# Kernel optimization log

Hardware: AMD Instinct MI355X
Metric: run time of the kernel (lower is better)

The kernel has to match this reference:

```python
import jax, jax.numpy as jnp
import numpy as np

ALPHA = 10.0 / 100.0  # dt / tau
HIDDEN_NOISE = 0.1
B, T, IN, H, OUT = 256, 200, 33, 2048, 4


def setup_inputs() -> dict:
    key = jax.random.key(0)
    k1, k2, k3, k4, k5 = jax.random.split(key, 5)
    x = jax.random.normal(k1, (B, T, IN), dtype=jnp.float32)
    # Pre-drawn per-step hidden noise (torch.normal(mean=0, std=hidden_noise)), shape [T, B, H]
    noise = jax.random.normal(k2, (T, B, H), dtype=jnp.float32) * HIDDEN_NOISE
    Wi2h = jax.random.normal(k3, (H, IN), dtype=jnp.float32) * (1.0 / np.sqrt(IN))
    Wrec = jax.random.normal(k4, (H, H), dtype=jnp.float32) * (1.0 / np.sqrt(H))
    Wh2o = jax.random.normal(k5, (OUT, H), dtype=jnp.float32) * (1.0 / np.sqrt(H))
    return {"x": x, "noise": noise, "Wi2h": Wi2h, "Wrec": Wrec, "Wh2o": Wh2o}


def reference(x, noise, Wi2h, Wrec, Wh2o):
    # x: [B, T, IN]; noise: [T, B, H]; Wi2h: [H, IN]; Wrec: [H, H]; Wh2o: [OUT, H]
    b = x.shape[0]
    # Input projection for all timesteps at once: it = i2h(x[:, t, :])
    it_all = jnp.einsum('bti,hi->tbh', x, Wi2h)  # [T, B, H]
    h0 = jnp.zeros((b, Wrec.shape[0]), dtype=x.dtype)

    def step(h_prev, inp):
        it, nz = inp
        pre = it + h_prev @ Wrec.T + nz
        h = jax.nn.relu(pre) * ALPHA + (1.0 - ALPHA) * h_prev  # external = 0, no ceiling
        out = jax.nn.softmax(h @ Wh2o.T, axis=1)
        return h, (h, out)

    _, (hs, outs) = jax.lax.scan(step, h0, (it_all, noise))
    hiddens = jnp.swapaxes(hs, 0, 1)   # [B, T, H]
    outs = jnp.swapaxes(outs, 0, 1)    # [B, T, OUT]
    return hiddens, outs
```

## Files before the change

### kernel.cpp

```cpp
#include <hip/hip_runtime.h>
#include <math.h>

#define Bq 256
#define Tq 200
#define INq 33
#define Hq 2048
#define OUTq 4

typedef __attribute__((ext_vector_type(8))) short bf16x8;
typedef __attribute__((ext_vector_type(16))) float f32x16;
typedef __attribute__((ext_vector_type(4))) unsigned short us4;

#define MFMA32(A, B, C) __builtin_amdgcn_mfma_f32_32x32x16_bf16((A), (B), (C), 0, 0, 0)

__device__ __forceinline__ unsigned short f32_to_bf16(float f) {
  unsigned u = __float_as_uint(f);
  unsigned r = 0x7FFFu + ((u >> 16) & 1u);
  return (unsigned short)((u + r) >> 16);
}
__device__ __forceinline__ float bf16_to_f32(unsigned short h) {
  return __uint_as_float((unsigned)h << 16);
}

#define WS_W1     0ull
#define WS_W2     8388608ull
#define WS_W3     16777216ull
#define WS_SLABF0 25165824ull
#define WS_SLABF1 27262976ull
#define WS_APARTS 29360128ull
#define WS_WIT    35651584ull
#define WS_TOTAL  35921920ull

#define DOT4(ACC, Av, Bv) \
  ACC = fmaf((Av).x, (Bv).x, ACC); ACC = fmaf((Av).y, (Bv).y, ACC); \
  ACC = fmaf((Av).z, (Bv).z, ACC); ACC = fmaf((Av).w, (Bv).w, ACC)

__global__ __launch_bounds__(256) void conv_wrec(
    const float* __restrict__ W, unsigned short* __restrict__ w1,
    unsigned short* __restrict__ w2, unsigned short* __restrict__ w3)
{
  const int g   = blockIdx.x * 256 + threadIdx.x;
  const int col = g >> 7;
  const int kc  = g & 127;
  const float* src = W + (size_t)col * Hq + kc * 16;
  unsigned short s1[16], s2[16], s3[16];
#pragma unroll
  for (int j = 0; j < 16; ++j) {
    float v = src[j];
    unsigned short b1 = f32_to_bf16(v);
    float r1 = v - bf16_to_f32(b1);
    unsigned short b2 = f32_to_bf16(r1);
    float r2 = r1 - bf16_to_f32(b2);
    s1[j] = b1; s2[j] = b2; s3[j] = f32_to_bf16(r2);
  }
  const size_t o_lo = ((size_t)(kc * 64 + (col >> 5)) * 64 + (col & 31)) * 8;
  const size_t o_hi = o_lo + 256;
#pragma unroll
  for (int jj = 0; jj < 2; ++jj) {
    *(us4*)&w1[o_lo + jj * 4] = *(us4*)&s1[jj * 4];
    *(us4*)&w1[o_hi + jj * 4] = *(us4*)&s1[8 + jj * 4];
    *(us4*)&w2[o_lo + jj * 4] = *(us4*)&s2[jj * 4];
    *(us4*)&w2[o_hi + jj * 4] = *(us4*)&s2[8 + jj * 4];
    *(us4*)&w3[o_lo + jj * 4] = *(us4*)&s3[jj * 4];
    *(us4*)&w3[o_hi + jj * 4] = *(us4*)&s3[8 + jj * 4];
  }
}

__global__ __launch_bounds__(256) void conv_wi(
    const float* __restrict__ Wi2h, float* __restrict__ WiT)
{
  const int g = blockIdx.x * 256 + threadIdx.x;
  if (g >= INq * Hq) return;
  const int i = g >> 11;
  const int c = g & 2047;
  WiT[(size_t)i * Hq + c] = Wi2h[(size_t)c * INq + i];
}

__global__ __launch_bounds__(256) void proj_tail(
    const float* __restrict__ hbase, size_t rstride,
    const float* __restrict__ Wh2o, float* __restrict__ out_o, int tp)
{
  const int tid = threadIdx.x;
  const int r  = blockIdx.x * 64 + (tid >> 2);
  const int p4 = tid & 3;
  const float* hp = hbase + (size_t)r * rstride;
  float a0 = 0.f, a1 = 0.f, a2 = 0.f, a3 = 0.f;
  const int k0 = p4 * 512;
#pragma unroll 4
  for (int k = k0; k < k0 + 512; k += 4) {
    float4 hv = *(const float4*)(hp + k);
    float4 w0 = *(const float4*)(Wh2o + 0 * Hq + k);
    float4 w1 = *(const float4*)(Wh2o + 1 * Hq + k);
    float4 w2 = *(const float4*)(Wh2o + 2 * Hq + k);
    float4 w3 = *(const float4*)(Wh2o + 3 * Hq + k);
    DOT4(a0, hv, w0); DOT4(a1, hv, w1); DOT4(a2, hv, w2); DOT4(a3, hv, w3);
  }
  a0 += __shfl_xor(a0, 1); a1 += __shfl_xor(a1, 1);
  a2 += __shfl_xor(a2, 1); a3 += __shfl_xor(a3, 1);
  a0 += __shfl_xor(a0, 2); a1 += __shfl_xor(a1, 2);
  a2 += __shfl_xor(a2, 2); a3 += __shfl_xor(a3, 2);
  if (p4 == 0) {
    float m  = fmaxf(fmaxf(a0, a1), fmaxf(a2, a3));
    float e0 = expf(a0 - m), e1 = expf(a1 - m);
    float e2 = expf(a2 - m), e3 = expf(a3 - m);
    float inv = 1.0f / (e0 + e1 + e2 + e3);
    float* op = out_o + ((size_t)r * Tq + tp) * OUTq;
    op[0] = e0 * inv; op[1] = e1 * inv; op[2] = e2 * inv; op[3] = e3 * inv;
  }
}

__global__ __launch_bounds__(512, 1) void rnn_step_mfma(
    const float* __restrict__ x, const float* __restrict__ noise,
    const float* __restrict__ WiT, const float* __restrict__ Wh2o,
    const unsigned short* __restrict__ w1, const unsigned short* __restrict__ w2,
    const unsigned short* __restrict__ w3,
    const float* __restrict__ hprevF,
    const unsigned short* __restrict__ a1, const unsigned short* __restrict__ a2,
    const unsigned short* __restrict__ a3,
    float* __restrict__ houtF,
    unsigned short* __restrict__ o1, unsigned short* __restrict__ o2,
    unsigned short* __restrict__ o3,
    float* __restrict__ out_h, float* __restrict__ out_o, int t)
{
  __shared__ float P[4 * 2176 + 32];

  const int wg  = blockIdx.x;
  const int tid = threadIdx.x;

  const int L  = (wg & 7) * 32 + (wg >> 3);
  const int TC = L >> 3;
  const int TR = L & 7;

  const int lane = tid & 63;
  const int wv   = __builtin_amdgcn_readfirstlane(tid >> 6);
  const int ct   = wv & 1;
  const int q    = wv >> 1;

  if (t > 0) {
    float* ps = P + 4 * 2176;
    const int i4 = tid * 4;
    float4 hv  = *(const float4*)(hprevF + (size_t)wg * Hq + i4);
    float4 q0v = *(const float4*)(Wh2o + 0 * Hq + i4);
    float4 q1v = *(const float4*)(Wh2o + 1 * Hq + i4);
    float4 q2v = *(const float4*)(Wh2o + 2 * Hq + i4);
    float4 q3v = *(const float4*)(Wh2o + 3 * Hq + i4);
    float s0 = 0.f, s1 = 0.f, s2 = 0.f, s3 = 0.f;
    DOT4(s0, hv, q0v); DOT4(s1, hv, q1v); DOT4(s2, hv, q2v); DOT4(s3, hv, q3v);
#pragma unroll
    for (int m = 1; m <= 32; m <<= 1) {
      s0 += __shfl_xor(s0, m); s1 += __shfl_xor(s1, m);
      s2 += __shfl_xor(s2, m); s3 += __shfl_xor(s3, m);
    }
    if ((tid & 63) == 0) {
      ps[wv * 4 + 0] = s0; ps[wv * 4 + 1] = s1;
      ps[wv * 4 + 2] = s2; ps[wv * 4 + 3] = s3;
    }
    __syncthreads();
    if (tid == 0) {
      float t0 = 0.f, t1 = 0.f, t2 = 0.f, t3 = 0.f;
#pragma unroll
      for (int w = 0; w < 8; ++w) {
        t0 += ps[w * 4 + 0]; t1 += ps[w * 4 + 1];
        t2 += ps[w * 4 + 2]; t3 += ps[w * 4 + 3];
      }
      float m  = fmaxf(fmaxf(t0, t1), fmaxf(t2, t3));
      float e0 = expf(t0 - m), e1 = expf(t1 - m);
      float e2 = expf(t2 - m), e3 = expf(t3 - m);
      float inv = 1.0f / (e0 + e1 + e2 + e3);
      float* op = out_o + ((size_t)wg * Tq + (t - 1)) * OUTq;
      op[0] = e0 * inv; op[1] = e1 * inv; op[2] = e2 * inv; op[3] = e3 * inv;
    }
    __syncthreads();
  }

  f32x16 accA, accB;
#pragma unroll
  for (int i = 0; i < 16; ++i) { accA[i] = 0.f; accB[i] = 0.f; }

  if (t > 0) {
    const int kc0 = q * 32;
    const unsigned short* pa1 = a1 + ((size_t)(kc0 * 8 + TR) * 64 + lane) * 8;
    const unsigned short* pa2 = a2 + ((size_t)(kc0 * 8 + TR) * 64 + lane) * 8;
    const unsigned short* pa3 = a3 + ((size_t)(kc0 * 8 + TR) * 64 + lane) * 8;
    const int cb = TC * 2 + ct;
    const unsigned short* pb1 = w1 + ((size_t)(kc0 * 64 + cb) * 64 + lane) * 8;
    const unsigned short* pb2 = w2 + ((size_t)(kc0 * 64 + cb) * 64 + lane) * 8;
    const unsigned short* pb3 = w3 + ((size_t)(kc0 * 64 + cb) * 64 + lane) * 8;

#define LA(P_, c) (*(const bf16x8*)((P_) + ((size_t)(c) << 12)))
#define LB(P_, c) (*(const bf16x8*)((P_) + ((size_t)(c) << 15)))
    bf16x8 A1x = LA(pa1, 0), A2x = LA(pa2, 0), A3x = LA(pa3, 0);
    bf16x8 B1x = LB(pb1, 0), B2x = LB(pb2, 0), B3x = LB(pb3, 0);
    bf16x8 A1y = LA(pa1, 1), A2y = LA(pa2, 1), A3y = LA(pa3, 1);
    bf16x8 B1y = LB(pb1, 1), B2y = LB(pb2, 1), B3y = LB(pb3, 1);

    for (int s = 0; s < 32; s += 2) {
      accA = MFMA32(A1x, B1x, accA);  accB = MFMA32(A2x, B1x, accB);
      accB = MFMA32(A1x, B2x, accB);  accA = MFMA32(A2x, B2x, accA);
      accA = MFMA32(A3x, B1x, accA);  accB = MFMA32(A1x, B3x, accB);
      accB = MFMA32(A3x, B2x, accB);  accA = MFMA32(A2x, B3x, accA);
      if (s + 2 < 32) {
        A1x = LA(pa1, s + 2); A2x = LA(pa2, s + 2); A3x = LA(pa3, s + 2);
        B1x = LB(pb1, s + 2); B2x = LB(pb2, s + 2); B3x = LB(pb3, s + 2);
      }
      accA = MFMA32(A1y, B1y, accA);  accB = MFMA32(A2y, B1y, accB);
      accB = MFMA32(A1y, B2y, accB);  accA = MFMA32(A2y, B2y, accA);
      accA = MFMA32(A3y, B1y, accA);  accB = MFMA32(A1y, B3y, accB);
      accB = MFMA32(A3y, B2y, accB);  accA = MFMA32(A2y, B3y, accA);
      if (s + 3 < 32) {
        A1y = LA(pa1, s + 3); A2y = LA(pa2, s + 3); A3y = LA(pa3, s + 3);
        B1y = LB(pb1, s + 3); B2y = LB(pb2, s + 3); B3y = LB(pb3, s + 3);
      }
    }
#undef LA
#undef LB

    const int prow0 = (lane >> 5) * 4;
    float* pw = P + q * 2176 + (ct * 32 + (lane & 31));
#pragma unroll
    for (int rr = 0; rr < 16; ++rr) {
      const int row = prow0 + (rr & 3) + 8 * (rr >> 2);
      pw[row * 68] = accA[rr] + accB[rr];
    }
  }
  __syncthreads();

  {
    const int row = tid >> 4;
    const int j0l = (tid & 15) * 4;
    const int b   = TR * 32 + row;
    const int gc  = TC * 64 + j0l;

    float e0 = 0.f, e1 = 0.f, e2 = 0.f, e3 = 0.f;
    if (t > 0) {
#pragma unroll
      for (int qq = 0; qq < 4; ++qq) {
        const float* pr = P + qq * 2176 + row * 68 + j0l;
        e0 += pr[0]; e1 += pr[1]; e2 += pr[2]; e3 += pr[3];
      }
    }

    const float* xb = x + ((size_t)b * Tq + t) * INq;
#pragma unroll
    for (int i = 0; i < INq; ++i) {
      float xv = xb[i];
      float4 wv4 = *(const float4*)(WiT + (size_t)i * Hq + gc);
      e0 = fmaf(xv, wv4.x, e0); e1 = fmaf(xv, wv4.y, e1);
      e2 = fmaf(xv, wv4.z, e2); e3 = fmaf(xv, wv4.w, e3);
    }

    float4 nz = *(const float4*)(noise + ((size_t)t * Bq + b) * Hq + gc);
    float4 hp = make_float4(0.f, 0.f, 0.f, 0.f);
    if (t > 0) hp = *(const float4*)(hprevF + (size_t)b * Hq + gc);

    float4 o;
    o.x = fmaf(fmaxf(e0 + nz.x, 0.f), 0.1f, 0.9f * hp.x);
    o.y = fmaf(fmaxf(e1 + nz.y, 0.f), 0.1f, 0.9f * hp.y);
    o.z = fmaf(fmaxf(e2 + nz.z, 0.f), 0.1f, 0.9f * hp.z);
    o.w = fmaf(fmaxf(e3 + nz.w, 0.f), 0.1f, 0.9f * hp.w);

    *(float4*)(out_h + ((size_t)b * Tq + t) * Hq + gc) = o;
    *(float4*)(houtF + (size_t)b * Hq + gc) = o;

    us4 p1v, p2v, p3v;
    float ov[4] = { o.x, o.y, o.z, o.w };
#pragma unroll
    for (int c = 0; c < 4; ++c) {
      unsigned short b1 = f32_to_bf16(ov[c]);
      float r1 = ov[c] - bf16_to_f32(b1);
      unsigned short b2 = f32_to_bf16(r1);
      float r2 = r1 - bf16_to_f32(b2);
      p1v[c] = b1; p2v[c] = b2; p3v[c] = f32_to_bf16(r2);
    }
    const size_t apo = ((size_t)((gc >> 4) * 8 + TR) * 64
                        + ((gc >> 3) & 1) * 32 + row) * 8 + (gc & 7);
    *(us4*)&o1[apo] = p1v;
    *(us4*)&o2[apo] = p2v;
    *(us4*)&o3[apo] = p3v;
  }
}

#define BKq 32
#define NST 16
__device__ __forceinline__ int swz(int row, int k) {
  return k ^ (((row >> 2) & 7) << 2);
}

template<bool SLAB>
__global__ __launch_bounds__(512, 2) void rnn_step(
    const float* __restrict__ x, const float* __restrict__ noise,
    const float* __restrict__ Wi2h, const float* __restrict__ Wrec,
    const float* __restrict__ Wh2o, float* __restrict__ out_h,
    float* __restrict__ out_o, const float* __restrict__ slabP,
    float* __restrict__ slabT, int t)
{
  constexpr size_t HSTR = SLAB ? (size_t)Hq : (size_t)Tq * Hq;
  __shared__ float smem[24576];
  const int wg  = blockIdx.x;
  const int tid = threadIdx.x;
  const int L  = (wg & 7) * 32 + (wg >> 3);
  const int TC = L >> 3;
  const int TR = L & 7;
  const int q  = tid >> 7;
  const int qt = tid & 127;
  const int tx = qt & 15;
  const int ty = qt >> 4;
  const int m0 = ty * 4, n0 = tx * 4;
  const int b0 = TR * 32 + m0;
  const int j0 = TC * 64 + n0;
  const int kb = q * 512;
  const float* hPrev = SLAB ? slabP : (out_h + (size_t)(t > 0 ? t - 1 : 0) * Hq);
  const int sm  = ((qt & 7) << 2) | ((qt >> 3) & 3);
  const int skh = ((qt >> 5) & 3) * 8;
  const int sn  = (((qt >> 5) & 1) << 5) | ((qt & 7) << 2) | ((qt >> 3) & 3);
  const int snk = ((qt >> 6) & 1) * 16;
  const float* gA = hPrev + (size_t)(TR * 32 + sm) * HSTR + kb + skh;
  const float* gB = Wrec + (size_t)(TC * 64 + sn) * Hq + kb + snk;
  float4 sA0, sA1, sB0, sB1, sB2, sB3;
  if (t > 0) {
    sA0 = *(const float4*)(gA);      sA1 = *(const float4*)(gA + 4);
    sB0 = *(const float4*)(gB);      sB1 = *(const float4*)(gB + 4);
    sB2 = *(const float4*)(gB + 8);  sB3 = *(const float4*)(gB + 12);
  }
  if (t > 0) {
    const int i4 = tid * 4;
    float4 hv = *(const float4*)(hPrev + (size_t)wg * HSTR + i4);
    float4 w0 = *(const float4*)(Wh2o + 0 * Hq + i4);
    float4 w1 = *(const float4*)(Wh2o + 1 * Hq + i4);
    float4 w2 = *(const float4*)(Wh2o + 2 * Hq + i4);
    float4 w3 = *(const float4*)(Wh2o + 3 * Hq + i4);
    float a0 = 0.f, a1 = 0.f, a2 = 0.f, a3 = 0.f;
    DOT4(a0, hv, w0); DOT4(a1, hv, w1); DOT4(a2, hv, w2); DOT4(a3, hv, w3);
#pragma unroll
    for (int m = 1; m <= 32; m <<= 1) {
      a0 += __shfl_xor(a0, m); a1 += __shfl_xor(a1, m);
      a2 += __shfl_xor(a2, m); a3 += __shfl_xor(a3, m);
    }
    if ((tid & 63) == 0) {
      const int w = tid >> 6;
      smem[w * 4 + 0] = a0; smem[w * 4 + 1] = a1;
      smem[w * 4 + 2] = a2; smem[w * 4 + 3] = a3;
    }
    __syncthreads();
    if (tid == 0) {
      float s0 = 0.f, s1 = 0.f, s2 = 0.f, s3 = 0.f;
#pragma unroll
      for (int w = 0; w < 8; ++w) {
        s0 += smem[w * 4 + 0]; s1 += smem[w * 4 + 1];
        s2 += smem[w * 4 + 2]; s3 += smem[w * 4 + 3];
      }
      float m  = fmaxf(fmaxf(s0, s1), fmaxf(s2, s3));
      float e0 = expf(s0 - m), e1 = expf(s1 - m);
      float e2 = expf(s2 - m), e3 = expf(s3 - m);
      float inv = 1.0f / (e0 + e1 + e2 + e3);
      float* op = out_o + ((size_t)wg * Tq + (t - 1)) * OUTq;
      op[0] = e0 * inv; op[1] = e1 * inv; op[2] = e2 * inv; op[3] = e3 * inv;
    }
    __syncthreads();
  }
  float acc00 = 0.f, acc01 = 0.f, acc02 = 0.f, acc03 = 0.f;
  float acc10 = 0.f, acc11 = 0.f, acc12 = 0.f, acc13 = 0.f;
  float acc20 = 0.f, acc21 = 0.f, acc22 = 0.f, acc23 = 0.f;
  float acc30 = 0.f, acc31 = 0.f, acc32 = 0.f, acc33 = 0.f;
  if (t > 0) {
    {
      float* aL = smem + q * 2048;
      float* bL = smem + 8192 + q * 4096;
      *(float4*)(aL + sm * 32 + swz(sm, skh))      = sA0;
      *(float4*)(aL + sm * 32 + swz(sm, skh + 4))  = sA1;
      *(float4*)(bL + sn * 32 + swz(sn, snk))      = sB0;
      *(float4*)(bL + sn * 32 + swz(sn, snk + 4))  = sB1;
      *(float4*)(bL + sn * 32 + swz(sn, snk + 8))  = sB2;
      *(float4*)(bL + sn * 32 + swz(sn, snk + 12)) = sB3;
    }
    __syncthreads();
    const int aKey = ty << 2;
    const int bKey = (tx & 7) << 2;
    for (int s = 0; s < NST; ++s) {
      const int buf = s & 1;
      if (s + 1 < NST) {
        const int o = (s + 1) * BKq;
        sA0 = *(const float4*)(gA + o);      sA1 = *(const float4*)(gA + o + 4);
        sB0 = *(const float4*)(gB + o);      sB1 = *(const float4*)(gB + o + 4);
        sB2 = *(const float4*)(gB + o + 8);  sB3 = *(const float4*)(gB + o + 12);
      }
      const float* aT = smem + q * 2048 + buf * 1024 + ty * 128;
      const float* bT = smem + 8192 + q * 4096 + buf * 2048 + tx * 128;
#pragma unroll
      for (int k4 = 0; k4 < BKq; k4 += 4) {
        const float* ap = aT + (k4 ^ aKey);
        const float* bp = bT + (k4 ^ bKey);
        float4 A0 = *(const float4*)(ap);
        float4 A1 = *(const float4*)(ap + 32);
        float4 A2 = *(const float4*)(ap + 64);
        float4 A3 = *(const float4*)(ap + 96);
        float4 Bv0 = *(const float4*)(bp);
        float4 Bv1 = *(const float4*)(bp + 32);
        float4 Bv2 = *(const float4*)(bp + 64);
        float4 Bv3 = *(const float4*)(bp + 96);
        DOT4(acc00, A0, Bv0); DOT4(acc01, A0, Bv1); DOT4(acc02, A0, Bv2); DOT4(acc03, A0, Bv3);
        DOT4(acc10, A1, Bv0); DOT4(acc11, A1, Bv1); DOT4(acc12, A1, Bv2); DOT4(acc13, A1, Bv3);
        DOT4(acc20, A2, Bv0); DOT4(acc21, A2, Bv1); DOT4(acc22, A2, Bv2); DOT4(acc23, A2, Bv3);
        DOT4(acc30, A3, Bv0); DOT4(acc31, A3, Bv1); DOT4(acc32, A3, Bv2); DOT4(acc33, A3, Bv3);
      }
      if (s + 1 < NST) {
        float* aL = smem + q * 2048 + (buf ^ 1) * 1024;
        float* bL = smem + 8192 + q * 4096 + (buf ^ 1) * 2048;
        *(float4*)(aL + sm * 32 + swz(sm, skh))      = sA0;
        *(float4*)(aL + sm * 32 + swz(sm, skh + 4))  = sA1;
        *(float4*)(bL + sn * 32 + swz(sn, snk))      = sB0;
        *(float4*)(bL + sn * 32 + swz(sn, snk + 4))  = sB1;
        *(float4*)(bL + sn * 32 + swz(sn, snk + 8))  = sB2;
        *(float4*)(bL + sn * 32 + swz(sn, snk + 12)) = sB3;
      }
      __syncthreads();
    }
  }
  {
    const int ilo = q * 8;
    const int ihi = (q == 3) ? INq : (ilo + 8);
    const float* xb = x + (size_t)b0 * Tq * INq + (size_t)t * INq;
    const float* wv = Wi2h + (size_t)j0 * INq;
    const size_t xs = (size_t)Tq * INq;
    for (int i = ilo; i < ihi; ++i) {
      float x0 = xb[i], x1 = xb[xs + i], x2 = xb[2 * xs + i], x3 = xb[3 * xs + i];
      float w0 = wv[i], w1 = wv[INq + i], w2 = wv[2 * INq + i], w3 = wv[3 * INq + i];
      acc00 = fmaf(x0, w0, acc00); acc01 = fmaf(x0, w1, acc01);
      acc02 = fmaf(x0, w2, acc02); acc03 = fmaf(x0, w3, acc03);
      acc10 = fmaf(x1, w0, acc10); acc11 = fmaf(x1, w1, acc11);
      acc12 = fmaf(x1, w2, acc12); acc13 = fmaf(x1, w3, acc13);
      acc20 = fmaf(x2, w0, acc20); acc21 = fmaf(x2, w1, acc21);
      acc22 = fmaf(x2, w2, acc22); acc23 = fmaf(x2, w3, acc23);
      acc30 = fmaf(x3, w0, acc30); acc31 = fmaf(x3, w1, acc31);
      acc32 = fmaf(x3, w2, acc32); acc33 = fmaf(x3, w3, acc33);
    }
  }
  if (q != 0) {
    float* rd = smem + (q - 1) * 2560 + qt * 20;
    *(float4*)(rd + 0)  = make_float4(acc00, acc01, acc02, acc03);
    *(float4*)(rd + 4)  = make_float4(acc10, acc11, acc12, acc13);
    *(float4*)(rd + 8)  = make_float4(acc20, acc21, acc22, acc23);
    *(float4*)(rd + 12) = make_float4(acc30, acc31, acc32, acc33);
  }
  __syncthreads();
  if (q == 0) {
#pragma unroll
    for (int p = 0; p < 3; ++p) {
      const float* rd = smem + p * 2560 + qt * 20;
      float4 r0 = *(const float4*)(rd + 0),  r1 = *(const float4*)(rd + 4);
      float4 r2 = *(const float4*)(rd + 8),  r3 = *(const float4*)(rd + 12);
      acc00 += r0.x; acc01 += r0.y; acc02 += r0.z; acc03 += r0.w;
      acc10 += r1.x; acc11 += r1.y; acc12 += r1.z; acc13 += r1.w;
      acc20 += r2.x; acc21 += r2.y; acc22 += r2.z; acc23 += r2.w;
      acc30 += r3.x; acc31 += r3.y; acc32 += r3.z; acc33 += r3.w;
    }
    const float* nzb = noise + ((size_t)t * Bq + b0) * Hq + j0;
    float4 nz0 = *(const float4*)(nzb);
    float4 nz1 = *(const float4*)(nzb + Hq);
    float4 nz2 = *(const float4*)(nzb + 2 * Hq);
    float4 nz3 = *(const float4*)(nzb + 3 * Hq);
    float4 hp0 = make_float4(0.f,0.f,0.f,0.f), hp1 = hp0, hp2 = hp0, hp3 = hp0;
    if (t > 0) {
      hp0 = *(const float4*)(hPrev + (size_t)(b0 + 0) * HSTR + j0);
      hp1 = *(const float4*)(hPrev + (size_t)(b0 + 1) * HSTR + j0);
      hp2 = *(const float4*)(hPrev + (size_t)(b0 + 2) * HSTR + j0);
      hp3 = *(const float4*)(hPrev + (size_t)(b0 + 3) * HSTR + j0);
    }
    float4 o0, o1, o2, o3;
    o0.x = fmaf(fmaxf(acc00 + nz0.x, 0.f), 0.1f, 0.9f * hp0.x);
    o0.y = fmaf(fmaxf(acc01 + nz0.y, 0.f), 0.1f, 0.9f * hp0.y);
    o0.z = fmaf(fmaxf(acc02 + nz0.z, 0.f), 0.1f, 0.9f * hp0.z);
    o0.w = fmaf(fmaxf(acc03 + nz0.w, 0.f), 0.1f, 0.9f * hp0.w);
    o1.x = fmaf(fmaxf(acc10 + nz1.x, 0.f), 0.1f, 0.9f * hp1.x);
    o1.y = fmaf(fmaxf(acc11 + nz1.y, 0.f), 0.1f, 0.9f * hp1.y);
    o1.z = fmaf(fmaxf(acc12 + nz1.z, 0.f), 0.1f, 0.9f * hp1.z);
    o1.w = fmaf(fmaxf(acc13 + nz1.w, 0.f), 0.1f, 0.9f * hp1.w);
    o2.x = fmaf(fmaxf(acc20 + nz2.x, 0.f), 0.1f, 0.9f * hp2.x);
    o2.y = fmaf(fmaxf(acc21 + nz2.y, 0.f), 0.1f, 0.9f * hp2.y);
    o2.z = fmaf(fmaxf(acc22 + nz2.z, 0.f), 0.1f, 0.9f * hp2.z);
    o2.w = fmaf(fmaxf(acc23 + nz2.w, 0.f), 0.1f, 0.9f * hp2.w);
    o3.x = fmaf(fmaxf(acc30 + nz3.x, 0.f), 0.1f, 0.9f * hp3.x);
    o3.y = fmaf(fmaxf(acc31 + nz3.y, 0.f), 0.1f, 0.9f * hp3.y);
    o3.z = fmaf(fmaxf(acc32 + nz3.z, 0.f), 0.1f, 0.9f * hp3.z);
    o3.w = fmaf(fmaxf(acc33 + nz3.w, 0.f), 0.1f, 0.9f * hp3.w);
    float* oh = out_h + (size_t)b0 * Tq * Hq + (size_t)t * Hq + j0;
    *(float4*)(oh)                       = o0;
    *(float4*)(oh + (size_t)Tq * Hq)     = o1;
    *(float4*)(oh + (size_t)2 * Tq * Hq) = o2;
    *(float4*)(oh + (size_t)3 * Tq * Hq) = o3;
    if (SLAB) {
      float* sl = slabT + (size_t)b0 * Hq + j0;
      *(float4*)(sl)            = o0;
      *(float4*)(sl + Hq)       = o1;
      *(float4*)(sl + 2 * Hq)   = o2;
      *(float4*)(sl + 3 * Hq)   = o3;
    }
  }
}

extern "C" void kernel_launch(void* const* d_in, const int* in_sizes, int n_in,
                              void* d_out, int out_size, void* d_ws, size_t ws_size,
                              hipStream_t stream) {
  const float* x     = (const float*)d_in[0];
  const float* noise = (const float*)d_in[1];
  const float* Wi2h  = (const float*)d_in[2];
  const float* Wrec  = (const float*)d_in[3];
  const float* Wh2o  = (const float*)d_in[4];
  float* out_h = (float*)d_out;
  float* out_o = out_h + (size_t)Bq * Tq * Hq;

  if (ws_size >= WS_TOTAL) {
    char* ws = (char*)d_ws;
    unsigned short* w1 = (unsigned short*)(ws + WS_W1);
    unsigned short* w2 = (unsigned short*)(ws + WS_W2);
    unsigned short* w3 = (unsigned short*)(ws + WS_W3);
    float* slabF[2] = { (float*)(ws + WS_SLABF0), (float*)(ws + WS_SLABF1) };
    float* WiT = (float*)(ws + WS_WIT);
    unsigned short* ap[2][3];
    for (int pp = 0; pp < 2; ++pp)
      for (int p = 0; p < 3; ++p)
        ap[pp][p] = (unsigned short*)(ws + WS_APARTS + ((size_t)(pp * 3 + p)) * 1048576ull);

    conv_wrec<<<1024, 256, 0, stream>>>(Wrec, w1, w2, w3);
    conv_wi<<<(INq * Hq + 255) / 256, 256, 0, stream>>>(Wi2h, WiT);

    for (int t = 0; t < Tq; ++t) {
      const int pc = t & 1;
      const int pp = pc ^ 1;
      rnn_step_mfma<<<256, 512, 0, stream>>>(
          x, noise, WiT, Wh2o, w1, w2, w3,
          slabF[pp], ap[pp][0], ap[pp][1], ap[pp][2],
          slabF[pc], ap[pc][0], ap[pc][1], ap[pc][2],
          out_h, out_o, t);
    }
    proj_tail<<<4, 256, 0, stream>>>(slabF[(Tq - 1) & 1], (size_t)Hq,
                                     Wh2o, out_o, Tq - 1);
  } else {
    const bool use_ws = ws_size >= (size_t)2 * Bq * Hq * sizeof(float);
    float* slab0 = (float*)d_ws;
    float* slab1 = slab0 + (size_t)Bq * Hq;
    if (use_ws) {
      for (int t = 0; t < Tq; ++t) {
        const float* sp = (t > 0) ? (((t - 1) & 1) ? slab1 : slab0) : nullptr;
        float*       st = (t & 1) ? slab1 : slab0;
        rnn_step<true><<<256, 512, 0, stream>>>(x, noise, Wi2h, Wrec, Wh2o,
                                                out_h, out_o, sp, st, t);
      }
      const float* hb = ((Tq - 1) & 1) ? slab1 : slab0;
      proj_tail<<<4, 256, 0, stream>>>(hb, (size_t)Hq, Wh2o, out_o, Tq - 1);
    } else {
      for (int t = 0; t < Tq; ++t) {
        rnn_step<false><<<256, 512, 0, stream>>>(x, noise, Wi2h, Wrec, Wh2o,
                                                 out_h, out_o, nullptr, nullptr, t);
      }
      proj_tail<<<4, 256, 0, stream>>>(out_h + (size_t)(Tq - 1) * Hq,
                                       (size_t)Tq * Hq, Wh2o, out_o, Tq - 1);
    }
  }
}
```

Baseline: 7.782 ms.

## Precompute input projection plus noise and drop low-order bf16 cross terms

Adds a make_pre kernel that computes x·Wi2hᵀ + noise for all timesteps up front into a large workspace buffer, so each recurrent step reads one float4 instead of running a 33-term dot product and a separate noise load. The per-step MFMA loop also drops the A3·B2 and A2·B3 terms of the split-bf16 product, cutting the matrix work per k-chunk from eight MFMAs to six at some cost in accuracy. The precompute path needs about 455MB of workspace and otherwise falls back to the old inline computation. The prologue is a serial loop over 256 batches with only 200 blocks, which adds its own latency.

Measured after the change: 8.876 ms. 1.14x slower.

```diff
diff --git a/kernel.cpp b/kernel.cpp
--- a/kernel.cpp
+++ b/kernel.cpp
@@ -30,6 +30,8 @@
 #define WS_APARTS 29360128ull
 #define WS_WIT    35651584ull
 #define WS_TOTAL  35921920ull
+#define WS_PRE    35921920ull
+#define WS_TOTAL_PRE 455352320ull
 
 #define DOT4(ACC, Av, Bv) \
   ACC = fmaf((Av).x, (Bv).x, ACC); ACC = fmaf((Av).y, (Bv).y, ACC); \
@@ -74,6 +76,26 @@
   const int i = g >> 11;
   const int c = g & 2047;
   WiT[(size_t)i * Hq + c] = Wi2h[(size_t)c * INq + i];
+}
+
+__global__ __launch_bounds__(512) void make_pre(
+    const float* __restrict__ x, const float* __restrict__ noise,
+    const float* __restrict__ WiT, float* __restrict__ pre)
+{
+  const int t  = blockIdx.x;
+  const int gc = threadIdx.x * 4;
+  for (int b = 0; b < Bq; ++b) {
+    const float* xb = x + ((size_t)b * Tq + t) * INq;
+    float4 acc = *(const float4*)(noise + ((size_t)t * Bq + b) * Hq + gc);
+#pragma unroll
+    for (int i = 0; i < INq; ++i) {
+      float xv = xb[i];
+      float4 wv = *(const float4*)(WiT + (size_t)i * Hq + gc);
+      acc.x = fmaf(xv, wv.x, acc.x); acc.y = fmaf(xv, wv.y, acc.y);
+      acc.z = fmaf(xv, wv.z, acc.z); acc.w = fmaf(xv, wv.w, acc.w);
+    }
+    *(float4*)(pre + ((size_t)t * Bq + b) * Hq + gc) = acc;
+  }
 }
 
 __global__ __launch_bounds__(256) void proj_tail(
@@ -109,9 +131,11 @@
   }
 }
 
+template<int MODE>
 __global__ __launch_bounds__(512, 1) void rnn_step_mfma(
     const float* __restrict__ x, const float* __restrict__ noise,
     const float* __restrict__ WiT, const float* __restrict__ Wh2o,
+    const float* __restrict__ preA,
     const unsigned short* __restrict__ w1, const unsigned short* __restrict__ w2,
     const unsigned short* __restrict__ w3,
     const float* __restrict__ hprevF,
@@ -196,17 +220,15 @@
 
     for (int s = 0; s < 32; s += 2) {
       accA = MFMA32(A1x, B1x, accA);  accB = MFMA32(A2x, B1x, accB);
-      accB = MFMA32(A1x, B2x, accB);  accA = MFMA32(A2x, B2x, accA);
+      accA = MFMA32(A2x, B2x, accA);  accB = MFMA32(A1x, B2x, accB);
       accA = MFMA32(A3x, B1x, accA);  accB = MFMA32(A1x, B3x, accB);
-      accB = MFMA32(A3x, B2x, accB);  accA = MFMA32(A2x, B3x, accA);
       if (s + 2 < 32) {
         A1x = LA(pa1, s + 2); A2x = LA(pa2, s + 2); A3x = LA(pa3, s + 2);
         B1x = LB(pb1, s + 2); B2x = LB(pb2, s + 2); B3x = LB(pb3, s + 2);
       }
       accA = MFMA32(A1y, B1y, accA);  accB = MFMA32(A2y, B1y, accB);
-      accB = MFMA32(A1y, B2y, accB);  accA = MFMA32(A2y, B2y, accA);
+      accA = MFMA32(A2y, B2y, accA);  accB = MFMA32(A1y, B2y, accB);
       accA = MFMA32(A3y, B1y, accA);  accB = MFMA32(A1y, B3y, accB);
-      accB = MFMA32(A3y, B2y, accB);  accA = MFMA32(A2y, B3y, accA);
       if (s + 3 < 32) {
         A1y = LA(pa1, s + 3); A2y = LA(pa2, s + 3); A3y = LA(pa3, s + 3);
         B1y = LB(pb1, s + 3); B2y = LB(pb2, s + 3); B3y = LB(pb3, s + 3);
@@ -240,24 +262,30 @@
       }
     }
 
-    const float* xb = x + ((size_t)b * Tq + t) * INq;
-#pragma unroll
-    for (int i = 0; i < INq; ++i) {
-      float xv = xb[i];
-      float4 wv4 = *(const float4*)(WiT + (size_t)i * Hq + gc);
-      e0 = fmaf(xv, wv4.x, e0); e1 = fmaf(xv, wv4.y, e1);
-      e2 = fmaf(xv, wv4.z, e2); e3 = fmaf(xv, wv4.w, e3);
-    }
-
-    float4 nz = *(const float4*)(noise + ((size_t)t * Bq + b) * Hq + gc);
+    if (MODE == 1) {
+      float4 pv = *(const float4*)(preA + ((size_t)t * Bq + b) * Hq + gc);
+      e0 += pv.x; e1 += pv.y; e2 += pv.z; e3 += pv.w;
+    } else {
+      const float* xb = x + ((size_t)b * Tq + t) * INq;
+#pragma unroll
+      for (int i = 0; i < INq; ++i) {
+        float xv = xb[i];
+        float4 wv4 = *(const float4*)(WiT + (size_t)i * Hq + gc);
+        e0 = fmaf(xv, wv4.x, e0); e1 = fmaf(xv, wv4.y, e1);
+        e2 = fmaf(xv, wv4.z, e2); e3 = fmaf(xv, wv4.w, e3);
+      }
+      float4 nz = *(const float4*)(noise + ((size_t)t * Bq + b) * Hq + gc);
+      e0 += nz.x; e1 += nz.y; e2 += nz.z; e3 += nz.w;
+    }
+
     float4 hp = make_float4(0.f, 0.f, 0.f, 0.f);
     if (t > 0) hp = *(const float4*)(hprevF + (size_t)b * Hq + gc);
 
     float4 o;
-    o.x = fmaf(fmaxf(e0 + nz.x, 0.f), 0.1f, 0.9f * hp.x);
-    o.y = fmaf(fmaxf(e1 + nz.y, 0.f), 0.1f, 0.9f * hp.y);
-    o.z = fmaf(fmaxf(e2 + nz.z, 0.f), 0.1f, 0.9f * hp.z);
-    o.w = fmaf(fmaxf(e3 + nz.w, 0.f), 0.1f, 0.9f * hp.w);
+    o.x = fmaf(fmaxf(e0, 0.f), 0.1f, 0.9f * hp.x);
+    o.y = fmaf(fmaxf(e1, 0.f), 0.1f, 0.9f * hp.y);
+    o.z = fmaf(fmaxf(e2, 0.f), 0.1f, 0.9f * hp.z);
+    o.w = fmaf(fmaxf(e3, 0.f), 0.1f, 0.9f * hp.w);
 
     *(float4*)(out_h + ((size_t)b * Tq + t) * Hq + gc) = o;
     *(float4*)(houtF + (size_t)b * Hq + gc) = o;
@@ -516,6 +544,7 @@
     unsigned short* w3 = (unsigned short*)(ws + WS_W3);
     float* slabF[2] = { (float*)(ws + WS_SLABF0), (float*)(ws + WS_SLABF1) };
     float* WiT = (float*)(ws + WS_WIT);
+    float* pre = (float*)(ws + WS_PRE);
     unsigned short* ap[2][3];
     for (int pp = 0; pp < 2; ++pp)
       for (int p = 0; p < 3; ++p)
@@ -524,14 +553,26 @@
     conv_wrec<<<1024, 256, 0, stream>>>(Wrec, w1, w2, w3);
     conv_wi<<<(INq * Hq + 255) / 256, 256, 0, stream>>>(Wi2h, WiT);
 
-    for (int t = 0; t < Tq; ++t) {
-      const int pc = t & 1;
-      const int pp = pc ^ 1;
-      rnn_step_mfma<<<256, 512, 0, stream>>>(
-          x, noise, WiT, Wh2o, w1, w2, w3,
-          slabF[pp], ap[pp][0], ap[pp][1], ap[pp][2],
-          slabF[pc], ap[pc][0], ap[pc][1], ap[pc][2],
-          out_h, out_o, t);
+    const bool use_pre = ws_size >= WS_TOTAL_PRE;
+    if (use_pre) {
+      make_pre<<<Tq, 512, 0, stream>>>(x, noise, WiT, pre);
+      for (int t = 0; t < Tq; ++t) {
+        const int pc = t & 1, pp = pc ^ 1;
+        rnn_step_mfma<1><<<256, 512, 0, stream>>>(
+            x, noise, WiT, Wh2o, pre, w1, w2, w3,
+            slabF[pp], ap[pp][0], ap[pp][1], ap[pp][2],
+            slabF[pc], ap[pc][0], ap[pc][1], ap[pc][2],
+            out_h, out_o, t);
+      }
+    } else {
+      for (int t = 0; t < Tq; ++t) {
+        const int pc = t & 1, pp = pc ^ 1;
+        rnn_step_mfma<0><<<256, 512, 0, stream>>>(
+            x, noise, WiT, Wh2o, nullptr, w1, w2, w3,
+            slabF[pp], ap[pp][0], ap[pp][1], ap[pp][2],
+            slabF[pc], ap[pc][0], ap[pc][1], ap[pc][2],
+            out_h, out_o, t);
+      }
     }
     proj_tail<<<4, 256, 0, stream>>>(slabF[(Tq - 1) & 1], (size_t)Hq,
                                      Wh2o, out_o, Tq - 1);
```

## Replace per-timestep launches with a persistent cooperative kernel and grid barrier

Applied to the files above, without the earlier changes.

The 200 per-step kernel launches and the final projection tail launch are replaced by one cooperative kernel of 256 workgroups. It loops over timesteps and synchronises through an atomic counter barrier in the workspace, which conv_wi resets before the launch. The aim is to remove launch overhead and the drain/refill gaps between dependent steps. In exchange it relies on all 256 blocks being co-resident, and each step now pays for a spin-wait barrier with device-scope fences.

Measured after the change: 27.14 ms. +248.8%, slower.

```diff
diff --git a/kernel.cpp b/kernel.cpp
--- a/kernel.cpp
+++ b/kernel.cpp
@@ -29,7 +29,8 @@
 #define WS_SLABF1 27262976ull
 #define WS_APARTS 29360128ull
 #define WS_WIT    35651584ull
-#define WS_TOTAL  35921920ull
+#define WS_BAR    35921920ull
+#define WS_TOTAL  35921984ull
 
 #define DOT4(ACC, Av, Bv) \
   ACC = fmaf((Av).x, (Bv).x, ACC); ACC = fmaf((Av).y, (Bv).y, ACC); \
@@ -67,13 +68,219 @@
 }
 
 __global__ __launch_bounds__(256) void conv_wi(
-    const float* __restrict__ Wi2h, float* __restrict__ WiT)
+    const float* __restrict__ Wi2h, float* __restrict__ WiT,
+    unsigned* __restrict__ bar)
 {
   const int g = blockIdx.x * 256 + threadIdx.x;
+  if (g == 0) *bar = 0u;
   if (g >= INq * Hq) return;
   const int i = g >> 11;
   const int c = g & 2047;
   WiT[(size_t)i * Hq + c] = Wi2h[(size_t)c * INq + i];
+}
+
+__global__ __launch_bounds__(512, 1) void rnn_persist(
+    const float* __restrict__ x, const float* __restrict__ noise,
+    const float* __restrict__ WiT, const float* __restrict__ Wh2o,
+    const unsigned short* __restrict__ w1, const unsigned short* __restrict__ w2,
+    const unsigned short* __restrict__ w3,
+    float* __restrict__ slab0, float* __restrict__ slab1,
+    unsigned short* __restrict__ ap0_1, unsigned short* __restrict__ ap0_2,
+    unsigned short* __restrict__ ap0_3,
+    unsigned short* __restrict__ ap1_1, unsigned short* __restrict__ ap1_2,
+    unsigned short* __restrict__ ap1_3,
+    float* __restrict__ out_h, float* __restrict__ out_o,
+    unsigned* __restrict__ bar)
+{
+  __shared__ float P[4 * 2176 + 32];
+
+  const int wg  = blockIdx.x;
+  const int tid = threadIdx.x;
+
+  const int L  = (wg & 7) * 32 + (wg >> 3);
+  const int TC = L >> 3;
+  const int TR = L & 7;
+
+  const int lane = tid & 63;
+  const int wv   = __builtin_amdgcn_readfirstlane(tid >> 6);
+  const int ct   = wv & 1;
+  const int q    = wv >> 1;
+
+  for (int t = 0; t <= Tq; ++t) {
+    const int pc = t & 1;
+    const float* hprevF = pc ? slab0 : slab1;
+    float*       houtF  = pc ? slab1 : slab0;
+    const unsigned short* a1 = pc ? ap0_1 : ap1_1;
+    const unsigned short* a2 = pc ? ap0_2 : ap1_2;
+    const unsigned short* a3 = pc ? ap0_3 : ap1_3;
+    unsigned short* o1 = pc ? ap1_1 : ap0_1;
+    unsigned short* o2 = pc ? ap1_2 : ap0_2;
+    unsigned short* o3 = pc ? ap1_3 : ap0_3;
+
+    if (t > 0) {
+      float* ps = P + 4 * 2176;
+      const int i4 = tid * 4;
+      float4 hv  = *(const float4*)(hprevF + (size_t)wg * Hq + i4);
+      float4 q0v = *(const float4*)(Wh2o + 0 * Hq + i4);
+      float4 q1v = *(const float4*)(Wh2o + 1 * Hq + i4);
+      float4 q2v = *(const float4*)(Wh2o + 2 * Hq + i4);
+      float4 q3v = *(const float4*)(Wh2o + 3 * Hq + i4);
+      float s0 = 0.f, s1 = 0.f, s2 = 0.f, s3 = 0.f;
+      DOT4(s0, hv, q0v); DOT4(s1, hv, q1v); DOT4(s2, hv, q2v); DOT4(s3, hv, q3v);
+#pragma unroll
+      for (int m = 1; m <= 32; m <<= 1) {
+        s0 += __shfl_xor(s0, m); s1 += __shfl_xor(s1, m);
+        s2 += __shfl_xor(s2, m); s3 += __shfl_xor(s3, m);
+      }
+      if ((tid & 63) == 0) {
+        ps[wv * 4 + 0] = s0; ps[wv * 4 + 1] = s1;
+        ps[wv * 4 + 2] = s2; ps[wv * 4 + 3] = s3;
+      }
+      __syncthreads();
+      if (tid == 0) {
+        float t0 = 0.f, t1 = 0.f, t2 = 0.f, t3 = 0.f;
+#pragma unroll
+        for (int w = 0; w < 8; ++w) {
+          t0 += ps[w * 4 + 0]; t1 += ps[w * 4 + 1];
+          t2 += ps[w * 4 + 2]; t3 += ps[w * 4 + 3];
+        }
+        float m  = fmaxf(fmaxf(t0, t1), fmaxf(t2, t3));
+        float e0 = expf(t0 - m), e1 = expf(t1 - m);
+        float e2 = expf(t2 - m), e3 = expf(t3 - m);
+        float inv = 1.0f / (e0 + e1 + e2 + e3);
+        float* op = out_o + ((size_t)wg * Tq + (t - 1)) * OUTq;
+        op[0] = e0 * inv; op[1] = e1 * inv; op[2] = e2 * inv; op[3] = e3 * inv;
+      }
+      __syncthreads();
+    }
+
+    if (t == Tq) break;
+
+    f32x16 accA, accB;
+#pragma unroll
+    for (int i = 0; i < 16; ++i) { accA[i] = 0.f; accB[i] = 0.f; }
+
+    if (t > 0) {
+      const int kc0 = q * 32;
+      const unsigned short* pa1 = a1 + ((size_t)(kc0 * 8 + TR) * 64 + lane) * 8;
+      const unsigned short* pa2 = a2 + ((size_t)(kc0 * 8 + TR) * 64 + lane) * 8;
+      const unsigned short* pa3 = a3 + ((size_t)(kc0 * 8 + TR) * 64 + lane) * 8;
+      const int cb = TC * 2 + ct;
+      const unsigned short* pb1 = w1 + ((size_t)(kc0 * 64 + cb) * 64 + lane) * 8;
+      const unsigned short* pb2 = w2 + ((size_t)(kc0 * 64 + cb) * 64 + lane) * 8;
+      const unsigned short* pb3 = w3 + ((size_t)(kc0 * 64 + cb) * 64 + lane) * 8;
+
+#define LA(P_, c) (*(const bf16x8*)((P_) + ((size_t)(c) << 12)))
+#define LB(P_, c) (*(const bf16x8*)((P_) + ((size_t)(c) << 15)))
+      bf16x8 A1x = LA(pa1, 0), A2x = LA(pa2, 0), A3x = LA(pa3, 0);
+      bf16x8 B1x = LB(pb1, 0), B2x = LB(pb2, 0), B3x = LB(pb3, 0);
+      bf16x8 A1y = LA(pa1, 1), A2y = LA(pa2, 1), A3y = LA(pa3, 1);
+      bf16x8 B1y = LB(pb1, 1), B2y = LB(pb2, 1), B3y = LB(pb3, 1);
+
+      for (int s = 0; s < 32; s += 2) {
+        accA = MFMA32(A1x, B1x, accA);  accB = MFMA32(A2x, B1x, accB);
+        accB = MFMA32(A1x, B2x, accB);  accA = MFMA32(A2x, B2x, accA);
+        accA = MFMA32(A3x, B1x, accA);  accB = MFMA32(A1x, B3x, accB);
+        accB = MFMA32(A3x, B2x, accB);  accA = MFMA32(A2x, B3x, accA);
+        if (s + 2 < 32) {
+          A1x = LA(pa1, s + 2); A2x = LA(pa2, s + 2); A3x = LA(pa3, s + 2);
+          B1x = LB(pb1, s + 2); B2x = LB(pb2, s + 2); B3x = LB(pb3, s + 2);
+        }
+        accA = MFMA32(A1y, B1y, accA);  accB = MFMA32(A2y, B1y, accB);
+        accB = MFMA32(A1y, B2y, accB);  accA = MFMA32(A2y, B2y, accA);
+        accA = MFMA32(A3y, B1y, accA);  accB = MFMA32(A1y, B3y, accB);
+        accB = MFMA32(A3y, B2y, accB);  accA = MFMA32(A2y, B3y, accA);
+        if (s + 3 < 32) {
+          A1y = LA(pa1, s + 3); A2y = LA(pa2, s + 3); A3y = LA(pa3, s + 3);
+          B1y = LB(pb1, s + 3); B2y = LB(pb2, s + 3); B3y = LB(pb3, s + 3);
+        }
+      }
+#undef LA
+#undef LB
+
+      const int prow0 = (lane >> 5) * 4;
+      float* pw = P + q * 2176 + (ct * 32 + (lane & 31));
+#pragma unroll
+      for (int rr = 0; rr < 16; ++rr) {
+        const int row = prow0 + (rr & 3) + 8 * (rr >> 2);
+        pw[row * 68] = accA[rr] + accB[rr];
+      }
+    }
+    __syncthreads();
+
+    {
+      const int row = tid >> 4;
+      const int j0l = (tid & 15) * 4;
+      const int b   = TR * 32 + row;
+      const int gc  = TC * 64 + j0l;
+
+      float e0 = 0.f, e1 = 0.f, e2 = 0.f, e3 = 0.f;
+      if (t > 0) {
+#pragma unroll
+        for (int qq = 0; qq < 4; ++qq) {
+          const float* pr = P + qq * 2176 + row * 68 + j0l;
+          e0 += pr[0]; e1 += pr[1]; e2 += pr[2]; e3 += pr[3];
+        }
+      }
+
+      const float* xb = x + ((size_t)b * Tq + t) * INq;
+#pragma unroll
+      for (int i = 0; i < INq; ++i) {
+        float xv = xb[i];
+        float4 wv4 = *(const float4*)(WiT + (size_t)i * Hq + gc);
+        e0 = fmaf(xv, wv4.x, e0); e1 = fmaf(xv, wv4.y, e1);
+        e2 = fmaf(xv, wv4.z, e2); e3 = fmaf(xv, wv4.w, e3);
+      }
+
+      float4 nz = *(const float4*)(noise + ((size_t)t * Bq + b) * Hq + gc);
+      e0 += nz.x; e1 += nz.y; e2 += nz.z; e3 += nz.w;
+
+      float4 hp = make_float4(0.f, 0.f, 0.f, 0.f);
+      if (t > 0) hp = *(const float4*)(hprevF + (size_t)b * Hq + gc);
+
+      float4 o;
+      o.x = fmaf(fmaxf(e0, 0.f), 0.1f, 0.9f * hp.x);
+      o.y = fmaf(fmaxf(e1, 0.f), 0.1f, 0.9f * hp.y);
+      o.z = fmaf(fmaxf(e2, 0.f), 0.1f, 0.9f * hp.z);
+      o.w = fmaf(fmaxf(e3, 0.f), 0.1f, 0.9f * hp.w);
+
+      *(float4*)(out_h + ((size_t)b * Tq + t) * Hq + gc) = o;
+      *(float4*)(houtF + (size_t)b * Hq + gc) = o;
+
+      us4 p1v, p2v, p3v;
+      float ov[4] = { o.x, o.y, o.z, o.w };
+#pragma unroll
+      for (int c = 0; c < 4; ++c) {
+        unsigned short b1 = f32_to_bf16(ov[c]);
+        float r1 = ov[c] - bf16_to_f32(b1);
+        unsigned short b2 = f32_to_bf16(r1);
+        float r2 = r1 - bf16_to_f32(b2);
+        p1v[c] = b1; p2v[c] = b2; p3v[c] = f32_to_bf16(r2);
+      }
+      const size_t apo = ((size_t)((gc >> 4) * 8 + TR) * 64
+                          + ((gc >> 3) & 1) * 32 + row) * 8 + (gc & 7);
+      *(us4*)&o1[apo] = p1v;
+      *(us4*)&o2[apo] = p2v;
+      *(us4*)&o3[apo] = p3v;
+    }
+
+    __threadfence();
+    __syncthreads();
+    if (tid == 0) {
+      __hip_atomic_fetch_add(bar, 1u, __ATOMIC_RELEASE, __HIP_MEMORY_SCOPE_AGENT);
+      const unsigned target = 256u * (unsigned)(t + 1);
+      while (__hip_atomic_load(bar, __ATOMIC_RELAXED, __HIP_MEMORY_SCOPE_AGENT) < target)
+        __builtin_amdgcn_s_sleep(1);
+    }
+    __syncthreads();
+    __threadfence();
+  }
+}
+
+#define BKq 32
+#define NST 16
+__device__ __forceinline__ int swz(int row, int k) {
+  return k ^ (((row >> 2) & 7) << 2);
 }
 
 __global__ __launch_bounds__(256) void proj_tail(
@@ -107,183 +314,6 @@
     float* op = out_o + ((size_t)r * Tq + tp) * OUTq;
     op[0] = e0 * inv; op[1] = e1 * inv; op[2] = e2 * inv; op[3] = e3 * inv;
   }
-}
-
-__global__ __launch_bounds__(512, 1) void rnn_step_mfma(
-    const float* __restrict__ x, const float* __restrict__ noise,
-    const float* __restrict__ WiT, const float* __restrict__ Wh2o,
-    const unsigned short* __restrict__ w1, const unsigned short* __restrict__ w2,
-    const unsigned short* __restrict__ w3,
-    const float* __restrict__ hprevF,
-    const unsigned short* __restrict__ a1, const unsigned short* __restrict__ a2,
-    const unsigned short* __restrict__ a3,
-    float* __restrict__ houtF,
-    unsigned short* __restrict__ o1, unsigned short* __restrict__ o2,
-    unsigned short* __restrict__ o3,
-    float* __restrict__ out_h, float* __restrict__ out_o, int t)
-{
-  __shared__ float P[4 * 2176 + 32];
-
-  const int wg  = blockIdx.x;
-  const int tid = threadIdx.x;
-
-  const int L  = (wg & 7) * 32 + (wg >> 3);
-  const int TC = L >> 3;
-  const int TR = L & 7;
-
-  const int lane = tid & 63;
-  const int wv   = __builtin_amdgcn_readfirstlane(tid >> 6);
-  const int ct   = wv & 1;
-  const int q    = wv >> 1;
-
-  if (t > 0) {
-    float* ps = P + 4 * 2176;
-    const int i4 = tid * 4;
-    float4 hv  = *(const float4*)(hprevF + (size_t)wg * Hq + i4);
-    float4 q0v = *(const float4*)(Wh2o + 0 * Hq + i4);
-    float4 q1v = *(const float4*)(Wh2o + 1 * Hq + i4);
-    float4 q2v = *(const float4*)(Wh2o + 2 * Hq + i4);
-    float4 q3v = *(const float4*)(Wh2o + 3 * Hq + i4);
-    float s0 = 0.f, s1 = 0.f, s2 = 0.f, s3 = 0.f;
-    DOT4(s0, hv, q0v); DOT4(s1, hv, q1v); DOT4(s2, hv, q2v); DOT4(s3, hv, q3v);
-#pragma unroll
-    for (int m = 1; m <= 32; m <<= 1) {
-      s0 += __shfl_xor(s0, m); s1 += __shfl_xor(s1, m);
-      s2 += __shfl_xor(s2, m); s3 += __shfl_xor(s3, m);
-    }
-    if ((tid & 63) == 0) {
-      ps[wv * 4 + 0] = s0; ps[wv * 4 + 1] = s1;
-      ps[wv * 4 + 2] = s2; ps[wv * 4 + 3] = s3;
-    }
-    __syncthreads();
-    if (tid == 0) {
-      float t0 = 0.f, t1 = 0.f, t2 = 0.f, t3 = 0.f;
-#pragma unroll
-      for (int w = 0; w < 8; ++w) {
-        t0 += ps[w * 4 + 0]; t1 += ps[w * 4 + 1];
-        t2 += ps[w * 4 + 2]; t3 += ps[w * 4 + 3];
-      }
-      float m  = fmaxf(fmaxf(t0, t1), fmaxf(t2, t3));
-      float e0 = expf(t0 - m), e1 = expf(t1 - m);
-      float e2 = expf(t2 - m), e3 = expf(t3 - m);
-      float inv = 1.0f / (e0 + e1 + e2 + e3);
-      float* op = out_o + ((size_t)wg * Tq + (t - 1)) * OUTq;
-      op[0] = e0 * inv; op[1] = e1 * inv; op[2] = e2 * inv; op[3] = e3 * inv;
-    }
-    __syncthreads();
-  }
-
-  f32x16 accA, accB;
-#pragma unroll
-  for (int i = 0; i < 16; ++i) { accA[i] = 0.f; accB[i] = 0.f; }
-
-  if (t > 0) {
-    const int kc0 = q * 32;
-    const unsigned short* pa1 = a1 + ((size_t)(kc0 * 8 + TR) * 64 + lane) * 8;
-    const unsigned short* pa2 = a2 + ((size_t)(kc0 * 8 + TR) * 64 + lane) * 8;
-    const unsigned short* pa3 = a3 + ((size_t)(kc0 * 8 + TR) * 64 + lane) * 8;
-    const int cb = TC * 2 + ct;
-    const unsigned short* pb1 = w1 + ((size_t)(kc0 * 64 + cb) * 64 + lane) * 8;
-    const unsigned short* pb2 = w2 + ((size_t)(kc0 * 64 + cb) * 64 + lane) * 8;
-    const unsigned short* pb3 = w3 + ((size_t)(kc0 * 64 + cb) * 64 + lane) * 8;
-
-#define LA(P_, c) (*(const bf16x8*)((P_) + ((size_t)(c) << 12)))
-#define LB(P_, c) (*(const bf16x8*)((P_) + ((size_t)(c) << 15)))
-    bf16x8 A1x = LA(pa1, 0), A2x = LA(pa2, 0), A3x = LA(pa3, 0);
-    bf16x8 B1x = LB(pb1, 0), B2x = LB(pb2, 0), B3x = LB(pb3, 0);
-    bf16x8 A1y = LA(pa1, 1), A2y = LA(pa2, 1), A3y = LA(pa3, 1);
-    bf16x8 B1y = LB(pb1, 1), B2y = LB(pb2, 1), B3y = LB(pb3, 1);
-
-    for (int s = 0; s < 32; s += 2) {
-      accA = MFMA32(A1x, B1x, accA);  accB = MFMA32(A2x, B1x, accB);
-      accB = MFMA32(A1x, B2x, accB);  accA = MFMA32(A2x, B2x, accA);
-      accA = MFMA32(A3x, B1x, accA);  accB = MFMA32(A1x, B3x, accB);
-      accB = MFMA32(A3x, B2x, accB);  accA = MFMA32(A2x, B3x, accA);
-      if (s + 2 < 32) {
-        A1x = LA(pa1, s + 2); A2x = LA(pa2, s + 2); A3x = LA(pa3, s + 2);
-        B1x = LB(pb1, s + 2); B2x = LB(pb2, s + 2); B3x = LB(pb3, s + 2);
-      }
-      accA = MFMA32(A1y, B1y, accA);  accB = MFMA32(A2y, B1y, accB);
-      accB = MFMA32(A1y, B2y, accB);  accA = MFMA32(A2y, B2y, accA);
-      accA = MFMA32(A3y, B1y, accA);  accB = MFMA32(A1y, B3y, accB);
-      accB = MFMA32(A3y, B2y, accB);  accA = MFMA32(A2y, B3y, accA);
-      if (s + 3 < 32) {
-        A1y = LA(pa1, s + 3); A2y = LA(pa2, s + 3); A3y = LA(pa3, s + 3);
-        B1y = LB(pb1, s + 3); B2y = LB(pb2, s + 3); B3y = LB(pb3, s + 3);
-      }
-    }
-#undef LA
-#undef LB
-
-    const int prow0 = (lane >> 5) * 4;
-    float* pw = P + q * 2176 + (ct * 32 + (lane & 31));
-#pragma unroll
-    for (int rr = 0; rr < 16; ++rr) {
-      const int row = prow0 + (rr & 3) + 8 * (rr >> 2);
-      pw[row * 68] = accA[rr] + accB[rr];
-    }
-  }
-  __syncthreads();
-
-  {
-    const int row = tid >> 4;
-    const int j0l = (tid & 15) * 4;
-    const int b   = TR * 32 + row;
-    const int gc  = TC * 64 + j0l;
-
-    float e0 = 0.f, e1 = 0.f, e2 = 0.f, e3 = 0.f;
-    if (t > 0) {
-#pragma unroll
-      for (int qq = 0; qq < 4; ++qq) {
-        const float* pr = P + qq * 2176 + row * 68 + j0l;
-        e0 += pr[0]; e1 += pr[1]; e2 += pr[2]; e3 += pr[3];
-      }
-    }
-
-    const float* xb = x + ((size_t)b * Tq + t) * INq;
-#pragma unroll
-    for (int i = 0; i < INq; ++i) {
-      float xv = xb[i];
-      float4 wv4 = *(const float4*)(WiT + (size_t)i * Hq + gc);
-      e0 = fmaf(xv, wv4.x, e0); e1 = fmaf(xv, wv4.y, e1);
-      e2 = fmaf(xv, wv4.z, e2); e3 = fmaf(xv, wv4.w, e3);
-    }
-
-    float4 nz = *(const float4*)(noise + ((size_t)t * Bq + b) * Hq + gc);
-    float4 hp = make_float4(0.f, 0.f, 0.f, 0.f);
-    if (t > 0) hp = *(const float4*)(hprevF + (size_t)b * Hq + gc);
-
-    float4 o;
-    o.x = fmaf(fmaxf(e0 + nz.x, 0.f), 0.1f, 0.9f * hp.x);
-    o.y = fmaf(fmaxf(e1 + nz.y, 0.f), 0.1f, 0.9f * hp.y);
-    o.z = fmaf(fmaxf(e2 + nz.z, 0.f), 0.1f, 0.9f * hp.z);
-    o.w = fmaf(fmaxf(e3 + nz.w, 0.f), 0.1f, 0.9f * hp.w);
-
-    *(float4*)(out_h + ((size_t)b * Tq + t) * Hq + gc) = o;
-    *(float4*)(houtF + (size_t)b * Hq + gc) = o;
-
-    us4 p1v, p2v, p3v;
-    float ov[4] = { o.x, o.y, o.z, o.w };
-#pragma unroll
-    for (int c = 0; c < 4; ++c) {
-      unsigned short b1 = f32_to_bf16(ov[c]);
-      float r1 = ov[c] - bf16_to_f32(b1);
-      unsigned short b2 = f32_to_bf16(r1);
-      float r2 = r1 - bf16_to_f32(b2);
-      p1v[c] = b1; p2v[c] = b2; p3v[c] = f32_to_bf16(r2);
-    }
-    const size_t apo = ((size_t)((gc >> 4) * 8 + TR) * 64
-                        + ((gc >> 3) & 1) * 32 + row) * 8 + (gc & 7);
-    *(us4*)&o1[apo] = p1v;
-    *(us4*)&o2[apo] = p2v;
-    *(us4*)&o3[apo] = p3v;
-  }
-}
-
-#define BKq 32
-#define NST 16
-__device__ __forceinline__ int swz(int row, int k) {
-  return k ^ (((row >> 2) & 7) << 2);
 }
 
 template<bool SLAB>
@@ -514,27 +544,27 @@
     unsigned short* w1 = (unsigned short*)(ws + WS_W1);
     unsigned short* w2 = (unsigned short*)(ws + WS_W2);
     unsigned short* w3 = (unsigned short*)(ws + WS_W3);
-    float* slabF[2] = { (float*)(ws + WS_SLABF0), (float*)(ws + WS_SLABF1) };
-    float* WiT = (float*)(ws + WS_WIT);
+    float* slab0 = (float*)(ws + WS_SLABF0);
+    float* slab1 = (float*)(ws + WS_SLABF1);
+    float* WiT   = (float*)(ws + WS_WIT);
+    unsigned* bar = (unsigned*)(ws + WS_BAR);
     unsigned short* ap[2][3];
     for (int pp = 0; pp < 2; ++pp)
       for (int p = 0; p < 3; ++p)
         ap[pp][p] = (unsigned short*)(ws + WS_APARTS + ((size_t)(pp * 3 + p)) * 1048576ull);
 
     conv_wrec<<<1024, 256, 0, stream>>>(Wrec, w1, w2, w3);
-    conv_wi<<<(INq * Hq + 255) / 256, 256, 0, stream>>>(Wi2h, WiT);
-
-    for (int t = 0; t < Tq; ++t) {
-      const int pc = t & 1;
-      const int pp = pc ^ 1;
-      rnn_step_mfma<<<256, 512, 0, stream>>>(
-          x, noise, WiT, Wh2o, w1, w2, w3,
-          slabF[pp], ap[pp][0], ap[pp][1], ap[pp][2],
-          slabF[pc], ap[pc][0], ap[pc][1], ap[pc][2],
-          out_h, out_o, t);
-    }
-    proj_tail<<<4, 256, 0, stream>>>(slabF[(Tq - 1) & 1], (size_t)Hq,
-                                     Wh2o, out_o, Tq - 1);
+    conv_wi<<<(INq * Hq + 255) / 256, 256, 0, stream>>>(Wi2h, WiT, bar);
+
+    void* args[] = { (void*)&x, (void*)&noise, (void*)&WiT, (void*)&Wh2o,
+                     (void*)&w1, (void*)&w2, (void*)&w3,
+                     (void*)&slab0, (void*)&slab1,
+                     (void*)&ap[0][0], (void*)&ap[0][1], (void*)&ap[0][2],
+                     (void*)&ap[1][0], (void*)&ap[1][1], (void*)&ap[1][2],
+                     (void*)&out_h, (void*)&out_o, (void*)&bar };
+    hipError_t err = hipLaunchCooperativeKernel((const void*)rnn_persist,
+                                                dim3(256), dim3(512), args, 0, stream);
+    (void)err;
   } else {
     const bool use_ws = ws_size >= (size_t)2 * Bq * Hq * sizeof(float);
     float* slab0 = (float*)d_ws;
```
